# Kernel tuning notes

Hardware: AMD Instinct MI355X
Metric: run time of the kernel (lower is better)

Reference implementation:

```python
import jax, jax.numpy as jnp
import numpy as np

N = 100000   # n_nodes
E = 1000000  # n_edges
B = 2000     # batch of interactions
K = 20       # n_neighbors
D = 172      # memory/node/edge/embedding dim
T = 172      # time encoding dim
MSG = 2 * D + D + T  # 688, identity message function
HEADS = 2


def setup_inputs() -> dict:
    key = jax.random.key(0)
    ks = jax.random.split(key, 32)
    g = lambda i, shape, fan: jax.random.normal(ks[i], shape, jnp.float32) / np.float32(np.sqrt(fan))
    inp = {}
    inp['memory'] = jax.random.normal(ks[0], (N, D), jnp.float32)
    inp['messages'] = jax.random.normal(ks[1], (N, MSG), jnp.float32)
    inp['edge_features'] = jax.random.normal(ks[2], (E, D), jnp.float32)
    inp['edge_times'] = jax.random.uniform(ks[3], (B,), jnp.float32) * 10000.0
    inp['neighbor_times'] = jax.random.uniform(ks[4], (3 * B, K), jnp.float32) * 10000.0
    # TimeEncode init: w = 1 / 10^linspace(0, 9, T)
    inp['time_w'] = jnp.asarray(1.0 / 10.0 ** np.linspace(0, 9, T), jnp.float32)
    inp['time_b'] = jnp.zeros((T,), jnp.float32)
    # GRUCell params
    inp['gru_w_ih'] = g(5, (3 * D, MSG), MSG)
    inp['gru_w_hh'] = g(6, (3 * D, D), D)
    inp['gru_b_ih'] = jnp.zeros((3 * D,), jnp.float32)
    inp['gru_b_hh'] = jnp.zeros((3 * D,), jnp.float32)
    # temporal attention params: query = [feat||time], key = [feat||edge||time]
    inp['w_q'] = g(7, (D, D + T), D + T)
    inp['w_k'] = g(8, (D, D + D + T), D + D + T)
    inp['w_v'] = g(9, (D, D + D + T), D + D + T)
    inp['w_o'] = g(10, (D, D), D)
    # MergeLayer(attn_out, src_feat)
    inp['merge_w1'] = g(11, (D, 2 * D), 2 * D)
    inp['merge_b1'] = jnp.zeros((D,), jnp.float32)
    inp['merge_w2'] = g(12, (D, D), D)
    inp['merge_b2'] = jnp.zeros((D,), jnp.float32)
    # affinity MergeLayer -> scalar score
    inp['aff_w1'] = g(13, (D, 2 * D), 2 * D)
    inp['aff_b1'] = jnp.zeros((D,), jnp.float32)
    inp['aff_w2'] = g(14, (1, D), D)
    inp['aff_b2'] = jnp.zeros((1,), jnp.float32)
    inp['source_nodes'] = jax.random.randint(ks[15], (B,), 0, N, jnp.int32)
    inp['destination_nodes'] = jax.random.randint(ks[16], (B,), 0, N, jnp.int32)
    inp['negative_nodes'] = jax.random.randint(ks[17], (B,), 0, N, jnp.int32)
    inp['neighbors'] = jax.random.randint(ks[18], (3 * B, K), 0, N, jnp.int32)
    inp['neighbor_edge_idxs'] = jax.random.randint(ks[19], (3 * B, K), 0, E, jnp.int32)
    return inp


def reference(memory, messages, edge_features, edge_times, neighbor_times,
              time_w, time_b, gru_w_ih, gru_w_hh, gru_b_ih, gru_b_hh,
              w_q, w_k, w_v, w_o, merge_w1, merge_b1, merge_w2, merge_b2,
              aff_w1, aff_b1, aff_w2, aff_b2,
              source_nodes, destination_nodes, negative_nodes,
              neighbors, neighbor_edge_idxs):
    d = memory.shape[1]
    dh = d // HEADS
    k_nbr = neighbors.shape[1]

    def time_enc(t):  # TimeEncode: cos(t * w + b)
        return jnp.cos(t[..., None] * time_w + time_b)

    # --- GRU memory update from aggregated ('last') messages ---
    gi = messages @ gru_w_ih.T + gru_b_ih          # [N, 3D]
    gh = memory @ gru_w_hh.T + gru_b_hh            # [N, 3D]
    i_r, i_z, i_n = jnp.split(gi, 3, axis=-1)
    h_r, h_z, h_n = jnp.split(gh, 3, axis=-1)
    r = jax.nn.sigmoid(i_r + h_r)
    z = jax.nn.sigmoid(i_z + h_z)
    n = jnp.tanh(i_n + r * h_n)
    mem_upd = (1.0 - z) * n + z * memory           # [N, D]

    # --- temporal graph attention embedding (1 layer) ---
    nodes = jnp.concatenate([source_nodes, destination_nodes, negative_nodes])  # [3B]
    ts = jnp.concatenate([edge_times, edge_times, edge_times])                  # [3B]
    m = nodes.shape[0]
    src_feat = mem_upd[nodes]                                                   # [3B, D]
    q_in = jnp.concatenate([src_feat, time_enc(jnp.zeros_like(ts))], axis=-1)   # [3B, D+T]
    nbr_feat = mem_upd[neighbors]                                               # [3B, K, D]
    e_feat = edge_features[neighbor_edge_idxs]                                  # [3B, K, D]
    dt = ts[:, None] - neighbor_times                                           # [3B, K]
    k_in = jnp.concatenate([nbr_feat, e_feat, time_enc(dt)], axis=-1)           # [3B, K, 2D+T]

    q = (q_in @ w_q.T).reshape(m, HEADS, dh)
    kk = (k_in @ w_k.T).reshape(m, k_nbr, HEADS, dh)
    vv = (k_in @ w_v.T).reshape(m, k_nbr, HEADS, dh)
    scores = jnp.einsum('nhd,nkhd->nhk', q, kk) / np.float32(np.sqrt(dh))
    valid = (neighbors > 0)[:, None, :]            # node 0 is the pad node
    scores = jnp.where(valid, scores, jnp.float32(-1e9))
    attn = jax.nn.softmax(scores, axis=-1)
    ctx = jnp.einsum('nhk,nkhd->nhd', attn, vv).reshape(m, d) @ w_o.T
    h1 = jax.nn.relu(jnp.concatenate([ctx, src_feat], axis=-1) @ merge_w1.T + merge_b1)
    emb = h1 @ merge_w2.T + merge_b2               # [3B, D]

    # --- affinity score on (src,dst) and (src,neg) pairs ---
    b = source_nodes.shape[0]
    s_emb, d_emb, n_emb = emb[:b], emb[b:2 * b], emb[2 * b:]
    s_cat = jnp.concatenate([s_emb, s_emb], axis=0)
    d_cat = jnp.concatenate([d_emb, n_emb], axis=0)
    ah = jax.nn.relu(jnp.concatenate([s_cat, d_cat], axis=-1) @ aff_w1.T + aff_b1)
    prob = jax.nn.sigmoid((ah @ aff_w2.T + aff_b2).squeeze(-1))  # [2B]
    return prob[:b], prob[b:]
```

## Files before the change

kernel.cpp:

```cpp
#include <hip/hip_runtime.h>
#include <math.h>

#define N_NODES 100000
#define BATCH   2000
#define KNBR    20
#define DF      172
#define MSGD    688
#define M3      6000
#define DH      86
#define KIN_D   516

#define KA      864
#define JP      768
#define KREAL   860
#define KSTEPS  (KA / 32)
#define NTILES_N ((N_NODES + 127) / 128)
#define NWG_GRU (NTILES_N * 6)

#define NKV     120000
#define KP_KV   544
#define JKV     384
#define KVS     352
#define NKV_TILES ((NKV + 127) / 128)
#define NKV_ROWS (NKV_TILES * 128)
#define NWG_KV  (NKV_TILES * 3)
#define KSTEPS_KV (KP_KV / 32)

typedef __bf16 bf16x8 __attribute__((ext_vector_type(8)));
typedef __bf16 bf16x4 __attribute__((ext_vector_type(4)));
typedef float  f32x4  __attribute__((ext_vector_type(4)));

#define WPB_OFF   0
#define BP4_OFF   331776
#define WKV_OFF   332544
#define MU_OFF    436992
#define UNI_OFF   17636992
#define KV_OFF    UNI_OFF
#define QB_OFF    38756992
#define CAT_OFF   39286400
#define EMBB_OFF  40922752
#define MW1O_OFF  41812608
#define WQB_OFF   41842192
#define WM1B_OFF  41875984
#define WM2B_OFF  41909776
#define WAFFB_OFF 41928208
#define BM1P_OFF  41962000
#define BM2P_OFF  41962192
#define BAFFP_OFF 41962384
#define NODES_OFF 41962768
#define KIN_OFF   42000000

__device__ __forceinline__ float sigmoidf_(float x) { return 1.0f / (1.0f + expf(-x)); }

typedef __attribute__((address_space(1))) const void gvoid;
typedef __attribute__((address_space(3))) void svoid;
__device__ __forceinline__ void gl16(const void* g, void* l) {
    __builtin_amdgcn_global_load_lds((gvoid*)g, (svoid*)l, 16, 0, 0);
}

__global__ __launch_bounds__(256) void prep_kernel(
    const float* __restrict__ w_ih, const float* __restrict__ w_hh,
    const float* __restrict__ b_ih, const float* __restrict__ b_hh,
    __bf16* __restrict__ wpb, float* __restrict__ bp4)
{
    int idx = blockIdx.x * 256 + threadIdx.x;
    if (idx < JP * KA) {
        int j = idx / KA, k = idx - j * KA;
        int d = j >> 2, g = j & 3;
        float v = 0.f;
        if (d < DF) {
            if (g == 0) {
                if (k < MSGD) v = w_ih[d * MSGD + k];
                else if (k < KREAL) v = w_hh[d * DF + (k - MSGD)];
            } else if (g == 1) {
                if (k < MSGD) v = w_ih[(d + DF) * MSGD + k];
                else if (k < KREAL) v = w_hh[(d + DF) * DF + (k - MSGD)];
            } else if (g == 2) {
                if (k < MSGD) v = w_ih[(d + 2 * DF) * MSGD + k];
            } else {
                if (k >= MSGD && k < KREAL) v = w_hh[(d + 2 * DF) * DF + (k - MSGD)];
            }
        }
        wpb[idx] = (__bf16)v;
    }
    if (idx < JP) {
        int d = idx >> 2, g = idx & 3;
        float b = 0.f;
        if (d < DF) {
            if (g == 0) b = b_ih[d] + b_hh[d];
            else if (g == 1) b = b_ih[d + DF] + b_hh[d + DF];
            else if (g == 2) b = b_ih[d + 2 * DF];
            else            b = b_hh[d + 2 * DF];
        }
        bp4[idx] = b;
    }
}

__global__ __launch_bounds__(256) void prep_kv_kernel(
    const float* __restrict__ w_k, const float* __restrict__ w_v,
    __bf16* __restrict__ wkvb)
{
    int idx = blockIdx.x * 256 + threadIdx.x;
    if (idx < JKV * KP_KV) {
        int j = idx / KP_KV, k = idx - j * KP_KV;
        float v = 0.f;
        if (k < KIN_D) {
            if (j < DF) v = w_k[j * KIN_D + k];
            else if (j >= 192 && j < 192 + DF) v = w_v[(j - 192) * KIN_D + k];
        }
        wkvb[idx] = (__bf16)v;
    }
}

__global__ __launch_bounds__(256) void conv_kernel(
    const float* __restrict__ messages, const float* __restrict__ memory,
    __bf16* __restrict__ xb)
{
    const long total = (long)N_NODES * (KA / 8);
    for (long idx = (long)blockIdx.x * 256 + threadIdx.x; idx < total;
         idx += (long)gridDim.x * 256) {
        const int r  = (int)(idx / (KA / 8));
        const int k  = (int)(idx - (long)r * (KA / 8)) * 8;
        float f[8];
        if (k < MSGD) {
            const float4 a = *(const float4*)(messages + (size_t)r * MSGD + k);
            const float4 b = *(const float4*)(messages + (size_t)r * MSGD + k + 4);
            f[0]=a.x; f[1]=a.y; f[2]=a.z; f[3]=a.w;
            f[4]=b.x; f[5]=b.y; f[6]=b.z; f[7]=b.w;
        } else {
            const int o = k - MSGD;
            const float4 a = *(const float4*)(memory + (size_t)r * DF + o);
            float4 b = make_float4(0.f, 0.f, 0.f, 0.f);
            if (o <= 164) b = *(const float4*)(memory + (size_t)r * DF + o + 4);
            f[0]=a.x; f[1]=a.y; f[2]=a.z; f[3]=a.w;
            f[4]=b.x; f[5]=b.y; f[6]=b.z; f[7]=b.w;
        }
        bf16x8 v;
#pragma unroll
        for (int j = 0; j < 8; ++j) v[j] = (__bf16)f[j];
        *(bf16x8*)(xb + (size_t)r * KA + k) = v;
    }
}

__global__ __launch_bounds__(256) void mw1o_kernel(
    const float* __restrict__ merge_w1, const float* __restrict__ w_o,
    float* __restrict__ mw1o)
{
    int idx = blockIdx.x * 256 + threadIdx.x;
    if (idx >= DF * DF) return;
    int j = idx / DF, k = idx - j * DF;
    float s = 0.f;
    for (int c = 0; c < DF; ++c)
        s = fmaf(merge_w1[j * 344 + c], w_o[c * DF + k], s);
    mw1o[idx] = s;
}

__global__ __launch_bounds__(256) void prep_tail_kernel(
    const float* __restrict__ w_q, const float* __restrict__ mw1o,
    const float* __restrict__ merge_w1, const float* __restrict__ merge_w2,
    const float* __restrict__ aff_w1,
    const float* __restrict__ merge_b1, const float* __restrict__ merge_b2,
    const float* __restrict__ aff_b1,
    const int* __restrict__ src_nodes, const int* __restrict__ dst_nodes,
    const int* __restrict__ neg_nodes,
    __bf16* __restrict__ wqb, __bf16* __restrict__ wm1b,
    __bf16* __restrict__ wm2b, __bf16* __restrict__ waffb,
    float* __restrict__ bm1p, float* __restrict__ bm2p,
    float* __restrict__ baffp, int* __restrict__ nodes_cat)
{
    int idx = blockIdx.x * 256 + threadIdx.x;
    if (idx < 192 * 352) {
        int j = idx / 352, k = idx - j * 352;
        float vq = 0.f, vm = 0.f, va = 0.f;
        if (j < DF) {
            if (k < DF) {
                vq = w_q[j * 344 + k];
                vm = mw1o[j * DF + k];
                va = aff_w1[j * 344 + k];
            } else if (k >= 176 && k < 348) {
                vq = w_q[j * 344 + 172 + (k - 176)];
                vm = merge_w1[j * 344 + 172 + (k - 176)];
                va = aff_w1[j * 344 + 172 + (k - 176)];
            }
        }
        wqb[idx] = (__bf16)vq;
        wm1b[idx] = (__bf16)vm;
        waffb[idx] = (__bf16)va;
    }
    if (idx < 192 * 192) {
        int j = idx / 192, k = idx - j * 192;
        wm2b[idx] = (__bf16)((j < DF && k < DF) ? merge_w2[j * DF + k] : 0.f);
    }
    if (idx < 192) {
        bm1p[idx]  = (idx < DF) ? merge_b1[idx] : 0.f;
        bm2p[idx]  = (idx < DF) ? merge_b2[idx] : 0.f;
        baffp[idx] = (idx < DF) ? aff_b1[idx] : 0.f;
    }
    if (idx < 6016) {
        int i = min(idx, M3 - 1);
        int node;
        if (i < BATCH)          node = src_nodes[i];
        else if (i < 2 * BATCH) node = dst_nodes[i - BATCH];
        else                    node = neg_nodes[i - 2 * BATCH];
        nodes_cat[idx] = node;
    }
}

__global__ __launch_bounds__(512) void gru_mfma5_kernel(
    const __bf16* __restrict__ xb, const __bf16* __restrict__ wpb,
    const float* __restrict__ bp4, __bf16* __restrict__ mem_upd)
{
    __shared__ __align__(16) __bf16 Ws[3][128 * 32];
    __shared__ __align__(16) __bf16 Xs[3][128 * 32];

    const int t    = threadIdx.x;
    const int w    = t >> 6, lane = t & 63;
    const int lo   = lane & 15, hi = lane >> 4;
    const int wm   = w & 1;
    const int wn   = w >> 1;

    const int orig = blockIdx.x;
    const int q = NWG_GRU >> 3, rr = NWG_GRU & 7;
    const int xcd = orig & 7, oidx = orig >> 3;
    const int wgid = (xcd < rr ? xcd * (q + 1) : rr * (q + 1) + (xcd - rr) * q) + oidx;
    const int m_tile = wgid % 6;
    const int n_tile = wgid / 6;
    const int n0 = n_tile * 128;
    const int j0 = m_tile * 128;

    const int srow  = lane >> 2;
    const int sslot = ((lane & 3) ^ ((srow >> 1) & 3)) * 8;

    f32x4 acc[4][2];
#pragma unroll
    for (int mi = 0; mi < 4; ++mi)
#pragma unroll
        for (int ni = 0; ni < 2; ++ni)
            acc[mi][ni] = (f32x4){0.f, 0.f, 0.f, 0.f};

    const __bf16* wbase = wpb + (size_t)j0 * KA;
    const __bf16* xbase = xb + (size_t)n0 * KA;

#define STAGE(buf, k0)                                                          \
    {                                                                           \
        const int lr = w * 16 + srow;                                           \
        gl16(wbase + (size_t)lr * KA + (k0) + sslot, &Ws[buf][(w * 16) * 32]);  \
        gl16(xbase + (size_t)lr * KA + (k0) + sslot, &Xs[buf][(w * 16) * 32]);  \
    }

    STAGE(0, 0);
    STAGE(1, 32);

    const int fsa = (hi ^ ((lo >> 1) & 3)) * 8;
    for (int ks = 0; ks < KSTEPS; ++ks) {
        if (ks < KSTEPS - 1) {
            asm volatile("s_waitcnt vmcnt(2)" ::: "memory");
        } else {
            asm volatile("s_waitcnt vmcnt(0)" ::: "memory");
        }
        __builtin_amdgcn_s_barrier();
        if (ks + 2 < KSTEPS) STAGE((ks + 2) % 3, (ks + 2) * 32);

        const int bi = ks % 3;
        bf16x8 af[4], bx_[2];
#pragma unroll
        for (int i = 0; i < 4; ++i)
            af[i]  = *(const bf16x8*)&Ws[bi][(wm * 64 + i * 16 + lo) * 32 + fsa];
#pragma unroll
        for (int i = 0; i < 2; ++i)
            bx_[i] = *(const bf16x8*)&Xs[bi][(wn * 32 + i * 16 + lo) * 32 + fsa];
#pragma unroll
        for (int mi = 0; mi < 4; ++mi)
#pragma unroll
            for (int ni = 0; ni < 2; ++ni)
                acc[mi][ni] = __builtin_amdgcn_mfma_f32_16x16x32_bf16(
                    af[mi], bx_[ni], acc[mi][ni], 0, 0, 0);
    }
#undef STAGE

    const int dbase = m_tile * 32 + wm * 16;
#pragma unroll
    for (int mi = 0; mi < 4; ++mi) {
        const int d = dbase + mi * 4 + hi;
        if (d >= DF) continue;
        const float4 b4 = *(const float4*)&bp4[4 * d];
#pragma unroll
        for (int ni = 0; ni < 2; ++ni) {
            const int n = n0 + wn * 32 + ni * 16 + lo;
            if (n >= N_NODES) continue;
            float sr  = acc[mi][ni][0] + b4.x;
            float sz  = acc[mi][ni][1] + b4.y;
            float gin = acc[mi][ni][2] + b4.z;
            float ghn = acc[mi][ni][3] + b4.w;
            float mem = (float)xb[(size_t)n * KA + MSGD + d];
            float rg  = sigmoidf_(sr);
            float zg  = sigmoidf_(sz);
            float nt  = tanhf(fmaf(rg, ghn, gin));
            mem_upd[(size_t)n * DF + d] = (__bf16)fmaf(zg, mem - nt, nt);
        }
    }
}

__global__ __launch_bounds__(256) void kin_build_kernel(
    const __bf16* __restrict__ mem_upd, const float* __restrict__ edge_features,
    const float* __restrict__ edge_times, const float* __restrict__ neighbor_times,
    const float* __restrict__ time_w, const float* __restrict__ time_b,
    const int* __restrict__ neighbors, const int* __restrict__ nbr_eidx,
    __bf16* __restrict__ kin)
{
    const long total = (long)NKV_ROWS * 136;
    for (long idx = (long)blockIdx.x * 256 + threadIdx.x; idx < total;
         idx += (long)gridDim.x * 256) {
        const int r  = (int)(idx / 136);
        const int c  = (int)(idx - (long)r * 136) * 4;
        const int rc = min(r, NKV - 1);
        bf16x4 o;
        if (c < DF) {
            const int nbr = neighbors[rc];
            o = *(const bf16x4*)(mem_upd + (size_t)nbr * DF + c);
        } else if (c < 2 * DF) {
            const int eidx = nbr_eidx[rc];
            const float4 v = *(const float4*)(edge_features + (size_t)eidx * DF + (c - DF));
            o[0] = (__bf16)v.x; o[1] = (__bf16)v.y;
            o[2] = (__bf16)v.z; o[3] = (__bf16)v.w;
        } else if (c < KIN_D) {
            const float dt = edge_times[(rc / KNBR) % BATCH] - neighbor_times[rc];
            const float4 tw = *(const float4*)(time_w + (c - 2 * DF));
            const float4 tb = *(const float4*)(time_b + (c - 2 * DF));
            o[0] = (__bf16)cosf(fmaf(dt, tw.x, tb.x));
            o[1] = (__bf16)cosf(fmaf(dt, tw.y, tb.y));
            o[2] = (__bf16)cosf(fmaf(dt, tw.z, tb.z));
            o[3] = (__bf16)cosf(fmaf(dt, tw.w, tb.w));
        } else {
            o[0] = o[1] = o[2] = o[3] = (__bf16)0.f;
        }
        *(bf16x4*)(kin + (size_t)r * KP_KV + c) = o;
    }
}

__global__ __launch_bounds__(512) void kv_gemm4_kernel(
    const __bf16* __restrict__ kin, const __bf16* __restrict__ wkvb,
    __bf16* __restrict__ kv)
{
    __shared__ __align__(16) __bf16 Ws[3][128 * 32];
    __shared__ __align__(16) __bf16 Xs[3][128 * 32];

    const int t    = threadIdx.x;
    const int w    = t >> 6, lane = t & 63;
    const int lo   = lane & 15, hi = lane >> 4;
    const int wm   = w & 1;
    const int wn   = w >> 1;

    const int orig = blockIdx.x;
    const int q = NWG_KV >> 3, rr = NWG_KV & 7;
    const int xcd = orig & 7, oidx = orig >> 3;
    const int wgid = (xcd < rr ? xcd * (q + 1) : rr * (q + 1) + (xcd - rr) * q) + oidx;
    const int m_tile = wgid % 3;
    const int n_tile = wgid / 3;
    const int n0 = n_tile * 128;
    const int j0 = m_tile * 128;

    const int srow  = lane >> 2;
    const int sslot = ((lane & 3) ^ ((srow >> 1) & 3)) * 8;

    f32x4 acc[4][2];
#pragma unroll
    for (int mi = 0; mi < 4; ++mi)
#pragma unroll
        for (int ni = 0; ni < 2; ++ni)
            acc[mi][ni] = (f32x4){0.f, 0.f, 0.f, 0.f};

    const __bf16* wbase = wkvb + (size_t)j0 * KP_KV;
    const __bf16* xbase = kin + (size_t)n0 * KP_KV;

#define STAGE(buf, k0)                                                           \
    {                                                                            \
        const int lr = w * 16 + srow;                                            \
        gl16(wbase + (size_t)lr * KP_KV + (k0) + sslot, &Ws[buf][(w * 16) * 32]);\
        gl16(xbase + (size_t)lr * KP_KV + (k0) + sslot, &Xs[buf][(w * 16) * 32]);\
    }

    STAGE(0, 0);
    STAGE(1, 32);

    const int fsa = (hi ^ ((lo >> 1) & 3)) * 8;
    for (int ks = 0; ks < KSTEPS_KV; ++ks) {
        if (ks < KSTEPS_KV - 1) {
            asm volatile("s_waitcnt vmcnt(2)" ::: "memory");
        } else {
            asm volatile("s_waitcnt vmcnt(0)" ::: "memory");
        }
        __builtin_amdgcn_s_barrier();
        if (ks + 2 < KSTEPS_KV) STAGE((ks + 2) % 3, (ks + 2) * 32);

        const int bi = ks % 3;
        bf16x8 af[4], bx_[2];
#pragma unroll
        for (int i = 0; i < 4; ++i)
            af[i]  = *(const bf16x8*)&Ws[bi][(wm * 64 + i * 16 + lo) * 32 + fsa];
#pragma unroll
        for (int i = 0; i < 2; ++i)
            bx_[i] = *(const bf16x8*)&Xs[bi][(wn * 32 + i * 16 + lo) * 32 + fsa];
#pragma unroll
        for (int mi = 0; mi < 4; ++mi)
#pragma unroll
            for (int ni = 0; ni < 2; ++ni)
                acc[mi][ni] = __builtin_amdgcn_mfma_f32_16x16x32_bf16(
                    af[mi], bx_[ni], acc[mi][ni], 0, 0, 0);
    }
#undef STAGE

#pragma unroll
    for (int mi = 0; mi < 4; ++mi) {
        const int jb = j0 + wm * 64 + mi * 16 + hi * 4;
        int off;
        if (jb + 3 < DF)                 off = jb;
        else if (jb >= 192 && jb < 361)  off = jb - 16;
        else continue;
#pragma unroll
        for (int ni = 0; ni < 2; ++ni) {
            const int n = n0 + wn * 32 + ni * 16 + lo;
            if (n >= NKV) continue;
            bf16x4 o;
            o[0] = (__bf16)acc[mi][ni][0];
            o[1] = (__bf16)acc[mi][ni][1];
            o[2] = (__bf16)acc[mi][ni][2];
            o[3] = (__bf16)acc[mi][ni][3];
            *(bf16x4*)(kv + (size_t)n * KVS + off) = o;
        }
    }
}

__global__ __launch_bounds__(256) void q_gemm_kernel(
    const __bf16* __restrict__ wqb, const __bf16* __restrict__ mem_upd,
    const float* __restrict__ time_b, const int* __restrict__ nodes_cat,
    __bf16* __restrict__ qbuf)
{
    __shared__ __align__(16) __bf16 Ws[192 * 32];
    __shared__ __align__(16) __bf16 Xs[128][32];

    const int t    = threadIdx.x;
    const int w    = t >> 6, lane = t & 63;
    const int lo   = lane & 15, hi = lane >> 4;
    const int wm   = w >> 1, wn = w & 1;
    const int n0   = blockIdx.x * 128;

    const int xrow  = t >> 1, xhalf = t & 1;
    const int nr    = min(n0 + xrow, M3 - 1);
    const __bf16* mrow = mem_upd + (size_t)nodes_cat[nr] * DF;

    const int srow  = lane >> 2;
    const int sslot = ((lane & 3) ^ ((srow >> 1) & 3)) * 8;
    const int fsa   = (hi ^ ((lo >> 1) & 3)) * 8;

    f32x4 acc[6][4];
#pragma unroll
    for (int mi = 0; mi < 6; ++mi)
#pragma unroll
        for (int ni = 0; ni < 4; ++ni)
            acc[mi][ni] = (f32x4){0.f, 0.f, 0.f, 0.f};

    for (int k0 = 0; k0 < 352; k0 += 32) {
#pragma unroll
        for (int qq = 0; qq < 3; ++qq) {
            const int jr = w * 48 + qq * 16 + srow;
            gl16(wqb + (size_t)jr * 352 + k0 + sslot, &Ws[(w * 48 + qq * 16) * 32]);
        }
        bf16x8 x0, x1;
#pragma unroll
        for (int c = 0; c < 4; ++c) {
            const int b = k0 + xhalf * 16 + c * 4;
            __bf16 e0, e1, e2, e3;
            if (b + 3 < DF) {
                bf16x4 h = *(const bf16x4*)(mrow + b);
                e0 = h[0]; e1 = h[1]; e2 = h[2]; e3 = h[3];
            } else if (b >= 176 && b < 348) {
                const float4 tb = *(const float4*)(time_b + (b - 176));
                e0 = (__bf16)cosf(tb.x); e1 = (__bf16)cosf(tb.y);
                e2 = (__bf16)cosf(tb.z); e3 = (__bf16)cosf(tb.w);
            } else {
                e0 = e1 = e2 = e3 = (__bf16)0.f;
            }
            if (c < 2) { x0[c*4]=e0; x0[c*4+1]=e1; x0[c*4+2]=e2; x0[c*4+3]=e3; }
            else { x1[(c-2)*4]=e0; x1[(c-2)*4+1]=e1; x1[(c-2)*4+2]=e2; x1[(c-2)*4+3]=e3; }
        }
        *(bf16x8*)&Xs[xrow][xhalf * 16]     = x0;
        *(bf16x8*)&Xs[xrow][xhalf * 16 + 8] = x1;
        __syncthreads();

        bf16x8 af[6], bx_[4];
#pragma unroll
        for (int i = 0; i < 6; ++i)
            af[i] = *(const bf16x8*)&Ws[(wm * 96 + i * 16 + lo) * 32 + fsa];
#pragma unroll
        for (int i = 0; i < 4; ++i)
            bx_[i] = *(const bf16x8*)&Xs[wn * 64 + i * 16 + lo][hi * 8];
#pragma unroll
        for (int mi = 0; mi < 6; ++mi)
#pragma unroll
            for (int ni = 0; ni < 4; ++ni)
                acc[mi][ni] = __builtin_amdgcn_mfma_f32_16x16x32_bf16(
                    af[mi], bx_[ni], acc[mi][ni], 0, 0, 0);
        __syncthreads();
    }

#pragma unroll
    for (int mi = 0; mi < 6; ++mi) {
        const int jb = wm * 96 + mi * 16 + hi * 4;
        if (jb + 3 >= 176) continue;
#pragma unroll
        for (int ni = 0; ni < 4; ++ni) {
            const int n = n0 + wn * 64 + ni * 16 + lo;
            if (n >= M3) continue;
            bf16x4 o;
            o[0]=(__bf16)acc[mi][ni][0]; o[1]=(__bf16)acc[mi][ni][1];
            o[2]=(__bf16)acc[mi][ni][2]; o[3]=(__bf16)acc[mi][ni][3];
            *(bf16x4*)(qbuf + (size_t)n * 176 + jb) = o;
        }
    }
}

__global__ __launch_bounds__(256) void attn_mid_kernel(
    const __bf16* __restrict__ mem_upd, const __bf16* __restrict__ kv,
    const __bf16* __restrict__ qb, const int* __restrict__ neighbors,
    const int* __restrict__ nodes_cat, __bf16* __restrict__ cat)
{
    __shared__ __align__(16) __bf16 kvs[2][KNBR][KVS];
    __shared__ float qs[2][176];
    __shared__ float scl[2][2][KNBR];
    __shared__ float attnl[2][2][KNBR];
    __shared__ int   nbrs[2][KNBR];

    const int i0 = blockIdx.x * 2;
    const int t = threadIdx.x;

    if (t < 2 * KNBR) {
        int q = t / KNBR, kn = t - q * KNBR;
        nbrs[q][kn] = neighbors[(i0 + q) * KNBR + kn];
    }
    for (int idx = t; idx < 352; idx += 256) {
        int q = idx / 176, c = idx - q * 176;
        qs[q][c] = (float)qb[(size_t)(i0 + q) * 176 + c];
    }
    {
        const uint4* src = (const uint4*)(kv + (size_t)i0 * KNBR * KVS);
        uint4* dst = (uint4*)&kvs[0][0][0];
        for (int idx = t; idx < 2 * KNBR * KVS / 8; idx += 256) dst[idx] = src[idx];
    }
    __syncthreads();

    if (t < 4 * KNBR) {
        int q = t / (2 * KNBR);
        int r = t - q * 2 * KNBR;
        int h = r / KNBR, kn = r - h * KNBR;
        float s = 0.f;
#pragma unroll 2
        for (int j = 0; j < DH; ++j)
            s = fmaf(qs[q][h * DH + j], (float)kvs[q][kn][h * DH + j], s);
        s /= sqrtf((float)DH);
        scl[q][h][kn] = (nbrs[q][kn] > 0) ? s : -1e9f;
    }
    __syncthreads();
    if (t < 4) {
        int q = t >> 1, h = t & 1;
        float m = -INFINITY;
        for (int kn = 0; kn < KNBR; ++kn) m = fmaxf(m, scl[q][h][kn]);
        float se = 0.f;
        for (int kn = 0; kn < KNBR; ++kn) se += expf(scl[q][h][kn] - m);
        float inv = 1.f / se;
        for (int kn = 0; kn < KNBR; ++kn)
            attnl[q][h][kn] = expf(scl[q][h][kn] - m) * inv;
    }
    __syncthreads();
    for (int idx = t; idx < 2 * DF; idx += 256) {
        int q = idx / DF, d = idx - q * DF;
        int h = d / DH;
        float cx = 0.f;
#pragma unroll
        for (int kn = 0; kn < KNBR; ++kn)
            cx = fmaf(attnl[q][h][kn], (float)kvs[q][kn][176 + d], cx);
        cat[(size_t)(i0 + q) * 352 + d] = (__bf16)cx;
        cat[(size_t)(i0 + q) * 352 + 176 + d] =
            mem_upd[(size_t)nodes_cat[i0 + q] * DF + d];
    }
    if (t < 8) {
        int q = t >> 2, r = t & 3;
        cat[(size_t)(i0 + q) * 352 + 172 + r] = (__bf16)0.f;
        cat[(size_t)(i0 + q) * 352 + 348 + r] = (__bf16)0.f;
    }
}

__global__ __launch_bounds__(256) void merge_emb_kernel(
    const __bf16* __restrict__ cat, const __bf16* __restrict__ wm1b,
    const __bf16* __restrict__ wm2b, const float* __restrict__ bm1p,
    const float* __restrict__ bm2p, __bf16* __restrict__ embb)
{
    __shared__ __align__(16) __bf16 Ws[192 * 32];
    __shared__ __align__(16) __bf16 Xs[64 * 32];
    __shared__ __align__(16) __bf16 h1[64 * 200];

    const int t    = threadIdx.x;
    const int w    = t >> 6, lane = t & 63;
    const int lo   = lane & 15, hi = lane >> 4;
    const int wm   = w >> 1, wn = w & 1;
    const int n0   = blockIdx.x * 64;

    const int srow  = lane >> 2;
    const int sslot = ((lane & 3) ^ ((srow >> 1) & 3)) * 8;
    const int fsa   = (hi ^ ((lo >> 1) & 3)) * 8;

    f32x4 acc[6][2];
#pragma unroll
    for (int mi = 0; mi < 6; ++mi)
#pragma unroll
        for (int ni = 0; ni < 2; ++ni)
            acc[mi][ni] = (f32x4){0.f, 0.f, 0.f, 0.f};

    for (int k0 = 0; k0 < 352; k0 += 32) {
#pragma unroll
        for (int qq = 0; qq < 3; ++qq) {
            const int jr = w * 48 + qq * 16 + srow;
            gl16(wm1b + (size_t)jr * 352 + k0 + sslot, &Ws[(w * 48 + qq * 16) * 32]);
        }
        {
            const int r = w * 16 + srow;
            const int nr = min(n0 + r, M3 - 1);
            gl16(cat + (size_t)nr * 352 + k0 + sslot, &Xs[(w * 16) * 32]);
        }
        asm volatile("s_waitcnt vmcnt(0)" ::: "memory");
        __syncthreads();

        bf16x8 af[6], bx_[2];
#pragma unroll
        for (int i = 0; i < 6; ++i)
            af[i] = *(const bf16x8*)&Ws[(wm * 96 + i * 16 + lo) * 32 + fsa];
#pragma unroll
        for (int i = 0; i < 2; ++i)
            bx_[i] = *(const bf16x8*)&Xs[(wn * 32 + i * 16 + lo) * 32 + fsa];
#pragma unroll
        for (int mi = 0; mi < 6; ++mi)
#pragma unroll
            for (int ni = 0; ni < 2; ++ni)
                acc[mi][ni] = __builtin_amdgcn_mfma_f32_16x16x32_bf16(
                    af[mi], bx_[ni], acc[mi][ni], 0, 0, 0);
        __syncthreads();
    }

#pragma unroll
    for (int mi = 0; mi < 6; ++mi) {
        const int jb = wm * 96 + mi * 16 + hi * 4;
        const float4 b4 = *(const float4*)(bm1p + jb);
#pragma unroll
        for (int ni = 0; ni < 2; ++ni) {
            const int nl = wn * 32 + ni * 16 + lo;
            bf16x4 o;
            o[0] = (__bf16)fmaxf(acc[mi][ni][0] + b4.x, 0.f);
            o[1] = (__bf16)fmaxf(acc[mi][ni][1] + b4.y, 0.f);
            o[2] = (__bf16)fmaxf(acc[mi][ni][2] + b4.z, 0.f);
            o[3] = (__bf16)fmaxf(acc[mi][ni][3] + b4.w, 0.f);
            *(bf16x4*)&h1[nl * 200 + jb] = o;
        }
    }
    __syncthreads();

    f32x4 acc2[6][2];
#pragma unroll
    for (int mi = 0; mi < 6; ++mi)
#pragma unroll
        for (int ni = 0; ni < 2; ++ni)
            acc2[mi][ni] = (f32x4){0.f, 0.f, 0.f, 0.f};

    for (int k0 = 0; k0 < 192; k0 += 32) {
#pragma unroll
        for (int qq = 0; qq < 3; ++qq) {
            const int jr = w * 48 + qq * 16 + srow;
            gl16(wm2b + (size_t)jr * 192 + k0 + sslot, &Ws[(w * 48 + qq * 16) * 32]);
        }
        asm volatile("s_waitcnt vmcnt(0)" ::: "memory");
        __syncthreads();

        bf16x8 af[6], bx_[2];
#pragma unroll
        for (int i = 0; i < 6; ++i)
            af[i] = *(const bf16x8*)&Ws[(wm * 96 + i * 16 + lo) * 32 + fsa];
#pragma unroll
        for (int i = 0; i < 2; ++i)
            bx_[i] = *(const bf16x8*)&h1[(wn * 32 + i * 16 + lo) * 200 + k0 + hi * 8];
#pragma unroll
        for (int mi = 0; mi < 6; ++mi)
#pragma unroll
            for (int ni = 0; ni < 2; ++ni)
                acc2[mi][ni] = __builtin_amdgcn_mfma_f32_16x16x32_bf16(
                    af[mi], bx_[ni], acc2[mi][ni], 0, 0, 0);
        __syncthreads();
    }

#pragma unroll
    for (int mi = 0; mi < 6; ++mi) {
        const int jb = wm * 96 + mi * 16 + hi * 4;
        if (jb + 3 >= 176) continue;
        const float4 b4 = *(const float4*)(bm2p + jb);
#pragma unroll
        for (int ni = 0; ni < 2; ++ni) {
            const int n = n0 + wn * 32 + ni * 16 + lo;
            if (n >= M3) continue;
            bf16x4 o;
            o[0] = (__bf16)(acc2[mi][ni][0] + b4.x);
            o[1] = (__bf16)(acc2[mi][ni][1] + b4.y);
            o[2] = (__bf16)(acc2[mi][ni][2] + b4.z);
            o[3] = (__bf16)(acc2[mi][ni][3] + b4.w);
            *(bf16x4*)(embb + (size_t)n * 176 + jb) = o;
        }
    }
}

__global__ __launch_bounds__(256) void aff_fused_kernel(
    const __bf16* __restrict__ embb, const __bf16* __restrict__ waffb,
    const float* __restrict__ baffp, const float* __restrict__ aff_w2,
    const float* __restrict__ aff_b2, float* __restrict__ out)
{
    __shared__ __align__(16) __bf16 Ws[192 * 32];
    __shared__ __align__(16) __bf16 Xs[128 * 32];
    __shared__ float sred[2][2][4][16];

    const int t    = threadIdx.x;
    const int w    = t >> 6, lane = t & 63;
    const int lo   = lane & 15, hi = lane >> 4;
    const int wm   = w >> 1, wn = w & 1;
    const int n0   = blockIdx.x * 128;

    const int srow  = lane >> 2;
    const int sslot = ((lane & 3) ^ ((srow >> 1) & 3)) * 8;
    const int fsa   = (hi ^ ((lo >> 1) & 3)) * 8;

    f32x4 acc[6][4];
#pragma unroll
    for (int mi = 0; mi < 6; ++mi)
#pragma unroll
        for (int ni = 0; ni < 4; ++ni)
            acc[mi][ni] = (f32x4){0.f, 0.f, 0.f, 0.f};

    for (int k0 = 0; k0 < 352; k0 += 32) {
#pragma unroll
        for (int qq = 0; qq < 3; ++qq) {
            const int jr = w * 48 + qq * 16 + srow;
            gl16(waffb + (size_t)jr * 352 + k0 + sslot, &Ws[(w * 48 + qq * 16) * 32]);
        }
#pragma unroll
        for (int qq = 0; qq < 2; ++qq) {
            const int r = w * 32 + qq * 16 + srow;
            const int nr = min(n0 + r, 2 * BATCH - 1);
            const int s  = (nr < BATCH) ? nr : nr - BATCH;
            const int col = k0 + sslot;
            const __bf16* src = (col < 176)
                ? embb + (size_t)s * 176 + col
                : embb + (size_t)(nr + BATCH) * 176 + (col - 176);
            gl16(src, &Xs[(w * 32 + qq * 16) * 32]);
        }
        asm volatile("s_waitcnt vmcnt(0)" ::: "memory");
        __syncthreads();

        bf16x8 af[6], bx_[4];
#pragma unroll
        for (int i = 0; i < 6; ++i)
            af[i] = *(const bf16x8*)&Ws[(wm * 96 + i * 16 + lo) * 32 + fsa];
#pragma unroll
        for (int i = 0; i < 4; ++i)
            bx_[i] = *(const bf16x8*)&Xs[(wn * 64 + i * 16 + lo) * 32 + fsa];
#pragma unroll
        for (int mi = 0; mi < 6; ++mi)
#pragma unroll
            for (int ni = 0; ni < 4; ++ni)
                acc[mi][ni] = __builtin_amdgcn_mfma_f32_16x16x32_bf16(
                    af[mi], bx_[ni], acc[mi][ni], 0, 0, 0);
        __syncthreads();
    }

    float ps[4] = {0.f, 0.f, 0.f, 0.f};
#pragma unroll
    for (int mi = 0; mi < 6; ++mi) {
        const int jb = wm * 96 + mi * 16 + hi * 4;
#pragma unroll
        for (int r = 0; r < 4; ++r) {
            const int j = jb + r;
            const float w2v = (j < DF) ? aff_w2[j] : 0.f;
            const float bb  = baffp[j];
#pragma unroll
            for (int ni = 0; ni < 4; ++ni)
                ps[ni] += fmaxf(acc[mi][ni][r] + bb, 0.f) * w2v;
        }
    }
#pragma unroll
    for (int ni = 0; ni < 4; ++ni) {
        ps[ni] += __shfl_xor(ps[ni], 16, 64);
        ps[ni] += __shfl_xor(ps[ni], 32, 64);
    }
    if (hi == 0) {
#pragma unroll
        for (int ni = 0; ni < 4; ++ni) sred[wm][wn][ni][lo] = ps[ni];
    }
    __syncthreads();
    if (t < 128) {
        const int n = n0 + t;
        if (n < 2 * BATCH) {
            const int wn2 = t >> 6, ni = (t >> 4) & 3, lo2 = t & 15;
            float s = sred[0][wn2][ni][lo2] + sred[1][wn2][ni][lo2] + aff_b2[0];
            out[n] = 1.f / (1.f + expf(-s));
        }
    }
}

extern "C" void kernel_launch(void* const* d_in, const int* in_sizes, int n_in,
                              void* d_out, int out_size, void* d_ws, size_t ws_size,
                              hipStream_t stream)
{
    (void)in_sizes; (void)n_in; (void)out_size; (void)ws_size;
    const float* memory         = (const float*)d_in[0];
    const float* messages       = (const float*)d_in[1];
    const float* edge_features  = (const float*)d_in[2];
    const float* edge_times     = (const float*)d_in[3];
    const float* neighbor_times = (const float*)d_in[4];
    const float* time_w         = (const float*)d_in[5];
    const float* time_b         = (const float*)d_in[6];
    const float* gru_w_ih       = (const float*)d_in[7];
    const float* gru_w_hh       = (const float*)d_in[8];
    const float* gru_b_ih       = (const float*)d_in[9];
    const float* gru_b_hh       = (const float*)d_in[10];
    const float* w_q            = (const float*)d_in[11];
    const float* w_k            = (const float*)d_in[12];
    const float* w_v            = (const float*)d_in[13];
    const float* w_o            = (const float*)d_in[14];
    const float* merge_w1       = (const float*)d_in[15];
    const float* merge_b1       = (const float*)d_in[16];
    const float* merge_w2       = (const float*)d_in[17];
    const float* merge_b2       = (const float*)d_in[18];
    const float* aff_w1         = (const float*)d_in[19];
    const float* aff_b1         = (const float*)d_in[20];
    const float* aff_w2         = (const float*)d_in[21];
    const float* aff_b2         = (const float*)d_in[22];
    const int* src_nodes        = (const int*)d_in[23];
    const int* dst_nodes        = (const int*)d_in[24];
    const int* neg_nodes        = (const int*)d_in[25];
    const int* neighbors        = (const int*)d_in[26];
    const int* nbr_eidx         = (const int*)d_in[27];

    float* ws       = (float*)d_ws;
    __bf16* wpb     = (__bf16*)(ws + WPB_OFF);
    float* bp4      = ws + BP4_OFF;
    __bf16* wkvb    = (__bf16*)(ws + WKV_OFF);
    __bf16* mem_upd = (__bf16*)(ws + MU_OFF);
    __bf16* xbuf    = (__bf16*)(ws + UNI_OFF);
    __bf16* kv      = (__bf16*)(ws + KV_OFF);
    __bf16* qbuf    = (__bf16*)(ws + QB_OFF);
    __bf16* cat     = (__bf16*)(ws + CAT_OFF);
    __bf16* embb    = (__bf16*)(ws + EMBB_OFF);
    float* mw1o     = ws + MW1O_OFF;
    __bf16* wqb     = (__bf16*)(ws + WQB_OFF);
    __bf16* wm1b    = (__bf16*)(ws + WM1B_OFF);
    __bf16* wm2b    = (__bf16*)(ws + WM2B_OFF);
    __bf16* waffb   = (__bf16*)(ws + WAFFB_OFF);
    float* bm1p     = ws + BM1P_OFF;
    float* bm2p     = ws + BM2P_OFF;
    float* baffp    = ws + BAFFP_OFF;
    int*   nodes_cat= (int*)(ws + NODES_OFF);
    __bf16* kin     = (__bf16*)(ws + KIN_OFF);
    float* out      = (float*)d_out;

    prep_kernel<<<(JP * KA + 255) / 256, 256, 0, stream>>>(
        gru_w_ih, gru_w_hh, gru_b_ih, gru_b_hh, wpb, bp4);
    prep_kv_kernel<<<(JKV * KP_KV + 255) / 256, 256, 0, stream>>>(w_k, w_v, wkvb);
    conv_kernel<<<2048, 256, 0, stream>>>(messages, memory, xbuf);
    gru_mfma5_kernel<<<NWG_GRU, 512, 0, stream>>>(xbuf, wpb, bp4, mem_upd);
    mw1o_kernel<<<(DF * DF + 255) / 256, 256, 0, stream>>>(merge_w1, w_o, mw1o);
    prep_tail_kernel<<<(192 * 352 + 255) / 256, 256, 0, stream>>>(
        w_q, mw1o, merge_w1, merge_w2, aff_w1, merge_b1, merge_b2, aff_b1,
        src_nodes, dst_nodes, neg_nodes,
        wqb, wm1b, wm2b, waffb, bm1p, bm2p, baffp, nodes_cat);
    kin_build_kernel<<<2048, 256, 0, stream>>>(
        mem_upd, edge_features, edge_times, neighbor_times, time_w, time_b,
        neighbors, nbr_eidx, kin);
    kv_gemm4_kernel<<<NWG_KV, 512, 0, stream>>>(kin, wkvb, kv);
    q_gemm_kernel<<<47, 256, 0, stream>>>(wqb, mem_upd, time_b, nodes_cat, qbuf);
    attn_mid_kernel<<<M3 / 2, 256, 0, stream>>>(
        mem_upd, kv, qbuf, neighbors, nodes_cat, cat);
    merge_emb_kernel<<<94, 256, 0, stream>>>(cat, wm1b, wm2b, bm1p, bm2p, embb);
    aff_fused_kernel<<<32, 256, 0, stream>>>(embb, waffb, baffp, aff_w2, aff_b2, out);
}
```

Baseline: 635.7 us.

## Restrict GRU memory update to nodes referenced by batch or neighbors

Adds flag, mark and compact kernels that build a list of the nodes actually referenced by the source, destination and negative batches or by the neighbor lists. The bf16 conversion gathers only those rows into a compacted buffer. The GRU GEMM early-exits tiles beyond the compacted count and scatters results back to the original node rows. This avoids computing memory updates for nodes no later stage reads, at the cost of three extra small launches, an atomic-based compaction with nondeterministic order, and gathered rather than streaming reads.

```diff
diff --git a/kernel.cpp b/kernel.cpp
--- a/kernel.cpp
+++ b/kernel.cpp
@@ -9,13 +9,14 @@
 #define M3      6000
 #define DH      86
 #define KIN_D   516
+#define NREFS   (3 * BATCH + NKV)
 
 #define KA      864
 #define JP      768
 #define KREAL   860
 #define KSTEPS  (KA / 32)
-#define NTILES_N ((N_NODES + 127) / 128)
-#define NWG_GRU (NTILES_N * 6)
+#define NTILES_MAX ((N_NODES + 127) / 128)
+#define NWG_GRU (NTILES_MAX * 6)
 
 #define NKV     120000
 #define KP_KV   544
@@ -49,6 +50,9 @@
 #define BAFFP_OFF 41962384
 #define NODES_OFF 41962768
 #define KIN_OFF   42000000
+#define FLAGS_OFF 74700000
+#define LIST_OFF  74800032
+#define CNT_OFF   74950000
 
 __device__ __forceinline__ float sigmoidf_(float x) { return 1.0f / (1.0f + expf(-x)); }
 
@@ -112,26 +116,62 @@
     }
 }
 
+__global__ __launch_bounds__(256) void flag_zero_kernel(
+    int* __restrict__ flags, int* __restrict__ cnt)
+{
+    int idx = blockIdx.x * 256 + threadIdx.x;
+    if (idx < N_NODES) flags[idx] = 0;
+    if (idx == 0) *cnt = 0;
+}
+
+__global__ __launch_bounds__(256) void flag_mark_kernel(
+    const int* __restrict__ src_nodes, const int* __restrict__ dst_nodes,
+    const int* __restrict__ neg_nodes, const int* __restrict__ neighbors,
+    int* __restrict__ flags)
+{
+    int idx = blockIdx.x * 256 + threadIdx.x;
+    if (idx >= NREFS) return;
+    int node;
+    if (idx < BATCH)          node = src_nodes[idx];
+    else if (idx < 2 * BATCH) node = dst_nodes[idx - BATCH];
+    else if (idx < 3 * BATCH) node = neg_nodes[idx - 2 * BATCH];
+    else                      node = neighbors[idx - 3 * BATCH];
+    flags[node] = 1;
+}
+
+__global__ __launch_bounds__(256) void compact_kernel(
+    const int* __restrict__ flags, int* __restrict__ list, int* __restrict__ cnt)
+{
+    int idx = blockIdx.x * 256 + threadIdx.x;
+    if (idx < N_NODES && flags[idx]) {
+        int pos = atomicAdd(cnt, 1);
+        list[pos] = idx;
+    }
+}
+
 __global__ __launch_bounds__(256) void conv_kernel(
     const float* __restrict__ messages, const float* __restrict__ memory,
+    const int* __restrict__ list, const int* __restrict__ cnt,
     __bf16* __restrict__ xb)
 {
-    const long total = (long)N_NODES * (KA / 8);
+    const int n = *cnt;
+    const long total = (long)n * (KA / 8);
     for (long idx = (long)blockIdx.x * 256 + threadIdx.x; idx < total;
          idx += (long)gridDim.x * 256) {
         const int r  = (int)(idx / (KA / 8));
         const int k  = (int)(idx - (long)r * (KA / 8)) * 8;
+        const int node = list[r];
         float f[8];
         if (k < MSGD) {
-            const float4 a = *(const float4*)(messages + (size_t)r * MSGD + k);
-            const float4 b = *(const float4*)(messages + (size_t)r * MSGD + k + 4);
+            const float4 a = *(const float4*)(messages + (size_t)node * MSGD + k);
+            const float4 b = *(const float4*)(messages + (size_t)node * MSGD + k + 4);
             f[0]=a.x; f[1]=a.y; f[2]=a.z; f[3]=a.w;
             f[4]=b.x; f[5]=b.y; f[6]=b.z; f[7]=b.w;
         } else {
             const int o = k - MSGD;
-            const float4 a = *(const float4*)(memory + (size_t)r * DF + o);
+            const float4 a = *(const float4*)(memory + (size_t)node * DF + o);
             float4 b = make_float4(0.f, 0.f, 0.f, 0.f);
-            if (o <= 164) b = *(const float4*)(memory + (size_t)r * DF + o + 4);
+            if (o <= 164) b = *(const float4*)(memory + (size_t)node * DF + o + 4);
             f[0]=a.x; f[1]=a.y; f[2]=a.z; f[3]=a.w;
             f[4]=b.x; f[5]=b.y; f[6]=b.z; f[7]=b.w;
         }
@@ -206,12 +246,16 @@
     }
 }
 
-__global__ __launch_bounds__(512) void gru_mfma5_kernel(
+__global__ __launch_bounds__(512) void gru_mfma6_kernel(
     const __bf16* __restrict__ xb, const __bf16* __restrict__ wpb,
-    const float* __restrict__ bp4, __bf16* __restrict__ mem_upd)
+    const float* __restrict__ bp4, const int* __restrict__ list,
+    const int* __restrict__ cnt, __bf16* __restrict__ mem_upd)
 {
     __shared__ __align__(16) __bf16 Ws[3][128 * 32];
     __shared__ __align__(16) __bf16 Xs[3][128 * 32];
+
+    const int cntv = *cnt;
+    const int ntiles = (cntv + 127) >> 7;
 
     const int t    = threadIdx.x;
     const int w    = t >> 6, lane = t & 63;
@@ -225,6 +269,7 @@
     const int wgid = (xcd < rr ? xcd * (q + 1) : rr * (q + 1) + (xcd - rr) * q) + oidx;
     const int m_tile = wgid % 6;
     const int n_tile = wgid / 6;
+    if (n_tile >= ntiles) return;
     const int n0 = n_tile * 128;
     const int j0 = m_tile * 128;
 
@@ -287,7 +332,8 @@
 #pragma unroll
         for (int ni = 0; ni < 2; ++ni) {
             const int n = n0 + wn * 32 + ni * 16 + lo;
-            if (n >= N_NODES) continue;
+            if (n >= cntv) continue;
+            const int node = list[n];
             float sr  = acc[mi][ni][0] + b4.x;
             float sz  = acc[mi][ni][1] + b4.y;
             float gin = acc[mi][ni][2] + b4.z;
@@ -296,7 +342,7 @@
             float rg  = sigmoidf_(sr);
             float zg  = sigmoidf_(sz);
             float nt  = tanhf(fmaf(rg, ghn, gin));
-            mem_upd[(size_t)n * DF + d] = (__bf16)fmaf(zg, mem - nt, nt);
+            mem_upd[(size_t)node * DF + d] = (__bf16)fmaf(zg, mem - nt, nt);
         }
     }
 }
@@ -864,13 +910,21 @@
     float* baffp    = ws + BAFFP_OFF;
     int*   nodes_cat= (int*)(ws + NODES_OFF);
     __bf16* kin     = (__bf16*)(ws + KIN_OFF);
+    int*   flags    = (int*)(ws + FLAGS_OFF);
+    int*   list     = (int*)(ws + LIST_OFF);
+    int*   cnt      = (int*)(ws + CNT_OFF);
     float* out      = (float*)d_out;
+
+    flag_zero_kernel<<<(N_NODES + 255) / 256, 256, 0, stream>>>(flags, cnt);
+    flag_mark_kernel<<<(NREFS + 255) / 256, 256, 0, stream>>>(
+        src_nodes, dst_nodes, neg_nodes, neighbors, flags);
+    compact_kernel<<<(N_NODES + 255) / 256, 256, 0, stream>>>(flags, list, cnt);
 
     prep_kernel<<<(JP * KA + 255) / 256, 256, 0, stream>>>(
         gru_w_ih, gru_w_hh, gru_b_ih, gru_b_hh, wpb, bp4);
     prep_kv_kernel<<<(JKV * KP_KV + 255) / 256, 256, 0, stream>>>(w_k, w_v, wkvb);
-    conv_kernel<<<2048, 256, 0, stream>>>(messages, memory, xbuf);
-    gru_mfma5_kernel<<<NWG_GRU, 512, 0, stream>>>(xbuf, wpb, bp4, mem_upd);
+    conv_kernel<<<2048, 256, 0, stream>>>(messages, memory, list, cnt, xbuf);
+    gru_mfma6_kernel<<<NWG_GRU, 512, 0, stream>>>(xbuf, wpb, bp4, list, cnt, mem_upd);
     mw1o_kernel<<<(DF * DF + 255) / 256, 256, 0, stream>>>(merge_w1, w_o, mw1o);
     prep_tail_kernel<<<(192 * 352 + 255) / 256, 256, 0, stream>>>(
         w_q, mw1o, merge_w1, merge_w2, aff_w1, merge_b1, merge_b2, aff_b1,
```

After: 639.1 us. Within noise of the previous version (+0.5%).
